# Optimization experiments

Hardware: AMD Instinct MI355X
Metric: run time of the kernel (lower is better)

## Reference

```python
import jax, jax.numpy as jnp
import numpy as np

EPS = 1e-3  # Keras BatchNormalization default epsilon

def _bn(x, g, b, m, v):
    return (x - m) * (g / jnp.sqrt(v + EPS)) + b

def _conv1d(x, w, b):
    # x: [B,T,Cin], w: [K,Cin,Cout], VALID padding
    y = jax.lax.conv_general_dilated(x, w, window_strides=(1,), padding='VALID',
                                     dimension_numbers=('NWC', 'WIO', 'NWC'))
    return y + b

def _lstm(x, W, U, b, return_sequences):
    # Keras LSTM: gates order [i, f, c, o]; sigmoid recurrent act, tanh act
    B, T, _ = x.shape
    H = U.shape[0]
    xz = jnp.einsum('btf,fh->bth', x, W) + b  # precompute input projection [B,T,4H]
    def step(carry, xz_t):
        h, c = carry
        z = xz_t + h @ U
        i, f, g, o = jnp.split(z, 4, axis=-1)
        i = jax.nn.sigmoid(i); f = jax.nn.sigmoid(f)
        g = jnp.tanh(g);       o = jax.nn.sigmoid(o)
        c = f * c + i * g
        h = o * jnp.tanh(c)
        return (h, c), h
    h0 = jnp.zeros((B, H), x.dtype)
    (h_last, _), hs = jax.lax.scan(step, (h0, h0), jnp.swapaxes(xz, 0, 1))
    return jnp.swapaxes(hs, 0, 1) if return_sequences else h_last

def setup_inputs() -> dict:
    key = jax.random.key(0)
    ks = jax.random.split(key, 32)
    B, T, F, C = 4096, 512, 10, 5
    s = 0.1
    d = {}
    d['x'] = jax.random.normal(ks[0], (B, T, F), jnp.float32)
    def bn(i, ch, p):
        d[p + '_g'] = jnp.ones((ch,), jnp.float32) + s * jax.random.normal(ks[i], (ch,))
        d[p + '_b'] = s * jax.random.normal(ks[i + 1], (ch,))
        d[p + '_m'] = s * jax.random.normal(ks[i + 2], (ch,))
        d[p + '_v'] = jnp.ones((ch,), jnp.float32) + 0.05 * jax.random.uniform(ks[i + 3], (ch,))
    bn(1, F, 'bn1'); bn(5, 16, 'bn2'); bn(9, 32, 'bn3')
    d['conv1_w'] = s * jax.random.normal(ks[13], (3, F, 16), jnp.float32)
    d['conv1_b'] = s * jax.random.normal(ks[14], (16,), jnp.float32)
    d['conv2_w'] = s * jax.random.normal(ks[15], (6, 16, 32), jnp.float32)
    d['conv2_b'] = s * jax.random.normal(ks[16], (32,), jnp.float32)
    def lstm_p(i, fin, h, p):
        d[p + '_W'] = s * jax.random.normal(ks[i], (fin, 4 * h), jnp.float32)
        d[p + '_U'] = s * jax.random.normal(ks[i + 1], (h, 4 * h), jnp.float32)
        d[p + '_b'] = s * jax.random.normal(ks[i + 2], (4 * h,), jnp.float32)
    lstm_p(17, 32, 32, 'l1'); lstm_p(20, 32, 24, 'l2'); lstm_p(23, 24, 16, 'l3')
    d['d1_w'] = s * jax.random.normal(ks[26], (16, 8), jnp.float32)
    d['d1_b'] = s * jax.random.normal(ks[27], (8,), jnp.float32)
    d['out_w'] = s * jax.random.normal(ks[28], (8, C), jnp.float32)
    d['out_b'] = s * jax.random.normal(ks[29], (C,), jnp.float32)
    return d

def reference(x, bn1_g, bn1_b, bn1_m, bn1_v, conv1_w, conv1_b,
              bn2_g, bn2_b, bn2_m, bn2_v, conv2_w, conv2_b,
              bn3_g, bn3_b, bn3_m, bn3_v,
              l1_W, l1_U, l1_b, l2_W, l2_U, l2_b, l3_W, l3_U, l3_b,
              d1_w, d1_b, out_w, out_b):
    # inference mode (training=False): BN uses moving stats, dropout is identity
    h = _bn(x, bn1_g, bn1_b, bn1_m, bn1_v)
    h = jax.nn.relu(_conv1d(h, conv1_w, conv1_b))
    h = _bn(h, bn2_g, bn2_b, bn2_m, bn2_v)
    h = jax.nn.relu(_conv1d(h, conv2_w, conv2_b))
    h = _bn(h, bn3_g, bn3_b, bn3_m, bn3_v)
    h = _lstm(h, l1_W, l1_U, l1_b, True)
    h = _lstm(h, l2_W, l2_U, l2_b, True)
    h = _lstm(h, l3_W, l3_U, l3_b, False)  # [B,16]
    h = jax.nn.relu(h @ d1_w + d1_b)
    return jax.nn.softmax(h @ out_w + out_b, axis=-1)
```

## Files before the change

kernel.cpp:

```cpp
#include <hip/hip_runtime.h>
#include <math.h>

#define EPSBN 1e-3f

typedef unsigned long long ull;
typedef __attribute__((ext_vector_type(8))) short bf16x8;
typedef __attribute__((ext_vector_type(4))) float f32x4;

#define WS_W1F 0
#define WS_B1F 480
#define WS_B2F 496
#define WS_W2F 528
#define WS_BL1 3600
#define WS_BL2 3728
#define WS_BL3 3824
#define WS_B1P 3888
#define WS_B2P 7984
#define WS_B3P 11056
#define WS_R2  13104

__device__ __forceinline__ unsigned short f2b(float f) {
  unsigned u = __float_as_uint(f);
  return (unsigned short)((u + 0x7FFFu + ((u >> 16) & 1u)) >> 16);
}
__device__ __forceinline__ float sigm(float v) { return 1.f / (1.f + __expf(-v)); }
__device__ __forceinline__ float tanh_(float v) {
  float e = __expf(-2.f * fabsf(v));
  float t = (1.f - e) / (1.f + e);
  return copysignf(t, v);
}

__global__ __launch_bounds__(256) void prep_kernel(
    const float* __restrict__ bn1g, const float* __restrict__ bn1b,
    const float* __restrict__ bn1m, const float* __restrict__ bn1v,
    const float* __restrict__ bn2g, const float* __restrict__ bn2b,
    const float* __restrict__ bn2m, const float* __restrict__ bn2v,
    const float* __restrict__ bn3g, const float* __restrict__ bn3b,
    const float* __restrict__ bn3m, const float* __restrict__ bn3v,
    const float* __restrict__ c1w, const float* __restrict__ c1b,
    const float* __restrict__ c2w, const float* __restrict__ c2b,
    const float* __restrict__ l1W, const float* __restrict__ l1U, const float* __restrict__ l1b,
    const float* __restrict__ l2W, const float* __restrict__ l2U, const float* __restrict__ l2b,
    const float* __restrict__ l3W, const float* __restrict__ l3U, const float* __restrict__ l3b,
    float* __restrict__ ws)
{
  __shared__ float s1[10], t1[10], s2[16], t2[16], s3[32], t3[32];
  int tid = threadIdx.x;
  if (tid < 10)                  { float s = bn1g[tid] * rsqrtf(bn1v[tid] + EPSBN); s1[tid] = s; t1[tid] = bn1b[tid] - bn1m[tid] * s; }
  else if (tid >= 32 && tid < 48){ int c = tid - 32; float s = bn2g[c] * rsqrtf(bn2v[c] + EPSBN); s2[c] = s; t2[c] = bn2b[c] - bn2m[c] * s; }
  else if (tid >= 64 && tid < 96){ int c = tid - 64; float s = bn3g[c] * rsqrtf(bn3v[c] + EPSBN); s3[c] = s; t3[c] = bn3b[c] - bn3m[c] * s; }
  __syncthreads();

  float* w1f = ws + WS_W1F;
  float* b1f = ws + WS_B1F;
  float* b2f = ws + WS_B2F;
  float* w2f = ws + WS_W2F;
  float* bL1 = ws + WS_BL1;
  float* bL2 = ws + WS_BL2;
  float* bL3 = ws + WS_BL3;
  unsigned short* B1P = (unsigned short*)(ws + WS_B1P);
  unsigned short* B2P = (unsigned short*)(ws + WS_B2P);
  unsigned short* B3P = (unsigned short*)(ws + WS_B3P);

  for (int i = tid; i < 480; i += 256) { int ci = (i >> 4) % 10; w1f[i] = c1w[i] * s1[ci]; }
  for (int co = tid; co < 16; co += 256) {
    float a = c1b[co];
    for (int k = 0; k < 3; k++) for (int ci = 0; ci < 10; ci++) a += t1[ci] * c1w[(k * 10 + ci) * 16 + co];
    b1f[co] = a;
  }
  for (int i = tid; i < 3072; i += 256) { int ci = (i >> 5) & 15; w2f[i] = c2w[i] * s2[ci]; }
  for (int co = tid; co < 32; co += 256) {
    float a = c2b[co];
    for (int k = 0; k < 6; k++) for (int ci = 0; ci < 16; ci++) a += t2[ci] * c2w[(k * 16 + ci) * 32 + co];
    b2f[co] = a;
  }
  for (int j = tid; j < 128; j += 256) {
    float a = l1b[j];
    for (int k = 0; k < 32; k++) a += t3[k] * l1W[k * 128 + j];
    bL1[j] = a;
  }
  for (int j = tid; j < 96; j += 256) bL2[j] = l2b[j];
  for (int j = tid; j < 64; j += 256) bL3[j] = l3b[j];

  for (int i = tid; i < 2 * 8 * 64 * 8; i += 256) {
    int e = i & 7, l = (i >> 3) & 63, nt = (i >> 9) & 7, kt = i >> 12;
    int j = nt * 16 + (l & 15);
    int k = kt * 32 + ((l >> 4) << 3) + e;
    float v = (k < 32) ? l1W[k * 128 + j] * s3[k] : l1U[(k - 32) * 128 + j];
    B1P[i] = f2b(v);
  }
  for (int i = tid; i < 2 * 6 * 64 * 8; i += 256) {
    int e = i & 7, l = (i >> 3) & 63, m = i >> 9;
    int nt = m % 6, kt = m / 6;
    int j = nt * 16 + (l & 15);
    int k = kt * 32 + ((l >> 4) << 3) + e;
    float v = (k < 32) ? l2W[k * 96 + j] : ((k < 56) ? l2U[(k - 32) * 96 + j] : 0.f);
    B2P[i] = f2b(v);
  }
  for (int i = tid; i < 2 * 4 * 64 * 8; i += 256) {
    int e = i & 7, l = (i >> 3) & 63, m = i >> 9;
    int nt = m & 3, kt = m >> 2;
    int j = nt * 16 + (l & 15);
    int k = kt * 32 + ((l >> 4) << 3) + e;
    float v = (k < 24) ? l3W[k * 64 + j] : ((k < 40) ? l3U[(k - 24) * 64 + j] : 0.f);
    B3P[i] = f2b(v);
  }
}

#define CT 128
__global__ __launch_bounds__(256, 4) void conv_kernel(
    const float* __restrict__ x, const float* __restrict__ ws,
    unsigned short* __restrict__ r2, int row0)
{
  int b  = row0 + blockIdx.y;
  int bl = blockIdx.y;
  int t0 = blockIdx.x * CT;
  int n2 = min(CT, 505 - t0);
  int n1 = n2 + 5;
  int nx = n1 + 2;
  int tid = threadIdx.x;

  __shared__ float xs[135 * 10];
  __shared__ float r1s[133 * 17];
  __shared__ float w1f[480];
  __shared__ float b1f[16];
  alignas(16) __shared__ float w2f[3072];
  __shared__ float b2f[32];

  for (int i = tid; i < 480;  i += 256) w1f[i] = ws[WS_W1F + i];
  for (int i = tid; i < 16;   i += 256) b1f[i] = ws[WS_B1F + i];
  for (int i = tid; i < 32;   i += 256) b2f[i] = ws[WS_B2F + i];
  for (int i = tid; i < 3072; i += 256) w2f[i] = ws[WS_W2F + i];
  const float* xb = x + (size_t)b * 512 * 10 + (size_t)t0 * 10;
  for (int i = tid; i < nx * 10; i += 256) xs[i] = xb[i];
  __syncthreads();

  #pragma unroll 1
  for (int i = tid; i < n1 * 16; i += 256) {
    int tt = i >> 4, c = i & 15;
    float a = b1f[c];
    #pragma unroll
    for (int k = 0; k < 3; k++)
      #pragma unroll
      for (int ci = 0; ci < 10; ci++)
        a = fmaf(xs[(tt + k) * 10 + ci], w1f[(k * 10 + ci) * 16 + c], a);
    r1s[tt * 17 + c] = fmaxf(a, 0.f);
  }
  __syncthreads();

  int cog = (tid & 7) * 4;
  int tg  = (tid >> 3) * 4;
  float acc[4][4];
  #pragma unroll
  for (int i2 = 0; i2 < 4; i2++)
    #pragma unroll
    for (int j2 = 0; j2 < 4; j2++) acc[i2][j2] = b2f[cog + j2];
  #pragma unroll 4
  for (int kc = 0; kc < 96; kc++) {
    int k2 = kc >> 4;
    float4 w4 = *(const float4*)&w2f[kc * 32 + cog];
    #pragma unroll
    for (int i2 = 0; i2 < 4; i2++) {
      float xv = r1s[(tg + i2 + k2) * 17 + (kc & 15)];
      acc[i2][0] = fmaf(xv, w4.x, acc[i2][0]);
      acc[i2][1] = fmaf(xv, w4.y, acc[i2][1]);
      acc[i2][2] = fmaf(xv, w4.z, acc[i2][2]);
      acc[i2][3] = fmaf(xv, w4.w, acc[i2][3]);
    }
  }
  #pragma unroll
  for (int i2 = 0; i2 < 4; i2++) {
    int tt = tg + i2;
    if (tt < n2) {
      ull o = (ull)f2b(fmaxf(acc[i2][0], 0.f))
            | ((ull)f2b(fmaxf(acc[i2][1], 0.f)) << 16)
            | ((ull)f2b(fmaxf(acc[i2][2], 0.f)) << 32)
            | ((ull)f2b(fmaxf(acc[i2][3], 0.f)) << 48);
      *(ull*)&r2[((size_t)bl * 505 + (t0 + tt)) * 32 + cog] = o;
    }
  }
}

#define SWZB(row, byte) ((byte) ^ (((row) & 7) << 4))
#define ZST 132

#define MFMA(a, b, c) __builtin_amdgcn_mfma_f32_16x16x32_bf16((a), (b), (c), 0, 0, 0)

__global__ __launch_bounds__(256) void lstm_kernel(
    const unsigned short* __restrict__ r2, const float* __restrict__ ws,
    const float* __restrict__ d1w, const float* __restrict__ d1b,
    const float* __restrict__ outw, const float* __restrict__ outb,
    float* __restrict__ out, int row0)
{
  int tid = threadIdx.x;
  int l   = tid & 63;
  int w   = tid >> 6;
  int r16 = l & 15;
  int g   = l >> 4;
  int rl  = blockIdx.x * 16;

  alignas(16) __shared__ unsigned short xh1[16 * 64];
  alignas(16) __shared__ unsigned short xh2[16 * 64];
  alignas(16) __shared__ unsigned short xh3[16 * 64];
  __shared__ float zbf[16 * ZST];

  const unsigned short* B1P = (const unsigned short*)(ws + WS_B1P);
  const unsigned short* B2P = (const unsigned short*)(ws + WS_B2P);
  const unsigned short* B3P = (const unsigned short*)(ws + WS_B3P);

  int nt1a = 2 * w, nt1b = 2 * w + 1;
  bool has2 = (w < 2);
  int nt2a = has2 ? 2 * w : (2 + w);
  int nt2b = has2 ? 2 * w + 1 : nt2a;
  bf16x8 B1r[2][2], B2r[2][2], B3r[2];
  #pragma unroll
  for (int kt = 0; kt < 2; kt++) {
    B1r[kt][0] = *(const bf16x8*)&B1P[((kt * 8 + nt1a) * 64 + l) * 8];
    B1r[kt][1] = *(const bf16x8*)&B1P[((kt * 8 + nt1b) * 64 + l) * 8];
    B2r[kt][0] = *(const bf16x8*)&B2P[((kt * 6 + nt2a) * 64 + l) * 8];
    B2r[kt][1] = *(const bf16x8*)&B2P[((kt * 6 + nt2b) * 64 + l) * 8];
    B3r[kt]    = *(const bf16x8*)&B3P[((kt * 4 + w) * 64 + l) * 8];
  }
  float b1a = ws[WS_BL1 + nt1a * 16 + r16];
  float b1b = ws[WS_BL1 + nt1b * 16 + r16];
  float b2a = ws[WS_BL2 + nt2a * 16 + r16];
  float b2b = ws[WS_BL2 + nt2b * 16 + r16];
  float b3  = ws[WS_BL3 + w * 16 + r16];

  int u1 = tid & 31, r1a = tid >> 5;
  int s2a = tid, r2a = s2a / 24, u2a = s2a - r2a * 24;
  int s2b = tid + 256, r2b = s2b / 24, u2b = s2b - r2b * 24;
  int u3 = tid & 15, r3a = tid >> 4;
  float c1A = 0.f, c1B = 0.f, c2A = 0.f, c2B = 0.f, c3 = 0.f;

  for (int i = tid; i < 16 * 64; i += 256) { xh1[i] = 0; xh2[i] = 0; xh3[i] = 0; }
  int xrow = tid >> 3, xch = tid & 7;
  const unsigned short* xp = r2 + ((size_t)(rl + xrow) * 505) * 32 + xch * 4;
  ull xreg = 0;
  if (tid < 128) xreg = *(const ull*)xp;
  __syncthreads();
  if (tid < 128) {
    *(ull*)((char*)xh1 + SWZB(xrow, xrow * 128 + xch * 8)) = xreg;
    xreg = *(const ull*)(xp + 32);
  }
  __syncthreads();

  #pragma unroll 1
  for (int t = 0; t < 505; ++t) {
    {
      bf16x8 a0 = *(const bf16x8*)((const char*)xh1 + SWZB(r16, r16 * 128 + g * 16));
      bf16x8 a1 = *(const bf16x8*)((const char*)xh1 + SWZB(r16, r16 * 128 + 64 + g * 16));
      f32x4 acc0 = {b1a, b1a, b1a, b1a};
      f32x4 acc1 = {b1b, b1b, b1b, b1b};
      acc0 = MFMA(a0, B1r[0][0], acc0);
      acc1 = MFMA(a0, B1r[0][1], acc1);
      acc0 = MFMA(a1, B1r[1][0], acc0);
      acc1 = MFMA(a1, B1r[1][1], acc1);
      int c0 = nt1a * 16 + r16, c1c = nt1b * 16 + r16;
      #pragma unroll
      for (int q = 0; q < 4; q++) {
        zbf[(g * 4 + q) * ZST + c0]  = acc0[q];
        zbf[(g * 4 + q) * ZST + c1c] = acc1[q];
      }
    }
    __syncthreads();
    if (tid < 128) {
      if (t < 504) *(ull*)((char*)xh1 + SWZB(xrow, xrow * 128 + xch * 8)) = xreg;
      if (t < 503) xreg = *(const ull*)(xp + (size_t)(t + 2) * 32);
    }
    {
      const float* z = &zbf[r1a * ZST];
      float gi = sigm(z[u1]), gf = sigm(z[32 + u1]), gg = tanh_(z[64 + u1]), go = sigm(z[96 + u1]);
      c1A = fmaf(gf, c1A, gi * gg);
      unsigned short hb = f2b(go * tanh_(c1A));
      *(unsigned short*)((char*)xh1 + SWZB(r1a, r1a * 128 + (32 + u1) * 2)) = hb;
      *(unsigned short*)((char*)xh2 + SWZB(r1a, r1a * 128 + u1 * 2)) = hb;
      int rB = r1a + 8;
      const float* zB = &zbf[rB * ZST];
      gi = sigm(zB[u1]); gf = sigm(zB[32 + u1]); gg = tanh_(zB[64 + u1]); go = sigm(zB[96 + u1]);
      c1B = fmaf(gf, c1B, gi * gg);
      hb = f2b(go * tanh_(c1B));
      *(unsigned short*)((char*)xh1 + SWZB(rB, rB * 128 + (32 + u1) * 2)) = hb;
      *(unsigned short*)((char*)xh2 + SWZB(rB, rB * 128 + u1 * 2)) = hb;
    }
    __syncthreads();
    {
      bf16x8 a0 = *(const bf16x8*)((const char*)xh2 + SWZB(r16, r16 * 128 + g * 16));
      bf16x8 a1 = *(const bf16x8*)((const char*)xh2 + SWZB(r16, r16 * 128 + 64 + g * 16));
      f32x4 acc0 = {b2a, b2a, b2a, b2a};
      acc0 = MFMA(a0, B2r[0][0], acc0);
      acc0 = MFMA(a1, B2r[1][0], acc0);
      int c0 = nt2a * 16 + r16;
      if (has2) {
        f32x4 acc1 = {b2b, b2b, b2b, b2b};
        acc1 = MFMA(a0, B2r[0][1], acc1);
        acc1 = MFMA(a1, B2r[1][1], acc1);
        int c1c = nt2b * 16 + r16;
        #pragma unroll
        for (int q = 0; q < 4; q++) {
          zbf[(g * 4 + q) * ZST + c0]  = acc0[q];
          zbf[(g * 4 + q) * ZST + c1c] = acc1[q];
        }
      } else {
        #pragma unroll
        for (int q = 0; q < 4; q++) zbf[(g * 4 + q) * ZST + c0] = acc0[q];
      }
    }
    __syncthreads();
    {
      const float* z = &zbf[r2a * ZST];
      float gi = sigm(z[u2a]), gf = sigm(z[24 + u2a]), gg = tanh_(z[48 + u2a]), go = sigm(z[72 + u2a]);
      c2A = fmaf(gf, c2A, gi * gg);
      unsigned short hb = f2b(go * tanh_(c2A));
      *(unsigned short*)((char*)xh2 + SWZB(r2a, r2a * 128 + (32 + u2a) * 2)) = hb;
      *(unsigned short*)((char*)xh3 + SWZB(r2a, r2a * 128 + u2a * 2)) = hb;
      if (tid < 128) {
        const float* zB = &zbf[r2b * ZST];
        gi = sigm(zB[u2b]); gf = sigm(zB[24 + u2b]); gg = tanh_(zB[48 + u2b]); go = sigm(zB[72 + u2b]);
        c2B = fmaf(gf, c2B, gi * gg);
        hb = f2b(go * tanh_(c2B));
        *(unsigned short*)((char*)xh2 + SWZB(r2b, r2b * 128 + (32 + u2b) * 2)) = hb;
        *(unsigned short*)((char*)xh3 + SWZB(r2b, r2b * 128 + u2b * 2)) = hb;
      }
    }
    __syncthreads();
    {
      bf16x8 a0 = *(const bf16x8*)((const char*)xh3 + SWZB(r16, r16 * 128 + g * 16));
      bf16x8 a1 = *(const bf16x8*)((const char*)xh3 + SWZB(r16, r16 * 128 + 64 + g * 16));
      f32x4 acc0 = {b3, b3, b3, b3};
      acc0 = MFMA(a0, B3r[0], acc0);
      acc0 = MFMA(a1, B3r[1], acc0);
      int c0 = w * 16 + r16;
      #pragma unroll
      for (int q = 0; q < 4; q++) zbf[(g * 4 + q) * ZST + c0] = acc0[q];
    }
    __syncthreads();
    {
      const float* z = &zbf[r3a * ZST];
      float gi = sigm(z[u3]), gf = sigm(z[16 + u3]), gg = tanh_(z[32 + u3]), go = sigm(z[48 + u3]);
      c3 = fmaf(gf, c3, gi * gg);
      float h = go * tanh_(c3);
      *(unsigned short*)((char*)xh3 + SWZB(r3a, r3a * 128 + (24 + u3) * 2)) = f2b(h);
      zbf[r3a * ZST + 64 + u3] = h;
    }
    __syncthreads();
  }

  if (tid < 16) {
    int row = tid;
    float hd[16];
    #pragma unroll
    for (int u = 0; u < 16; u++) hd[u] = zbf[row * ZST + 64 + u];
    float aa[8];
    #pragma unroll
    for (int o = 0; o < 8; o++) {
      float acc = d1b[o];
      #pragma unroll
      for (int u = 0; u < 16; u++) acc = fmaf(hd[u], d1w[u * 8 + o], acc);
      aa[o] = fmaxf(acc, 0.f);
    }
    float oo[5]; float mx = -1e30f;
    #pragma unroll
    for (int cc = 0; cc < 5; cc++) {
      float acc = outb[cc];
      #pragma unroll
      for (int o = 0; o < 8; o++) acc = fmaf(aa[o], outw[o * 5 + cc], acc);
      oo[cc] = acc; mx = fmaxf(mx, acc);
    }
    float sum = 0.f;
    #pragma unroll
    for (int cc = 0; cc < 5; cc++) { oo[cc] = __expf(oo[cc] - mx); sum += oo[cc]; }
    float inv = 1.f / sum;
    #pragma unroll
    for (int cc = 0; cc < 5; cc++) out[(size_t)(row0 + rl + row) * 5 + cc] = oo[cc] * inv;
  }
}

extern "C" void kernel_launch(void* const* d_in, const int* in_sizes, int n_in,
                              void* d_out, int out_size, void* d_ws, size_t ws_size,
                              hipStream_t stream)
{
  const float* x    = (const float*)d_in[0];
  const float* bn1g = (const float*)d_in[1];
  const float* bn1b = (const float*)d_in[2];
  const float* bn1m = (const float*)d_in[3];
  const float* bn1v = (const float*)d_in[4];
  const float* bn2g = (const float*)d_in[5];
  const float* bn2b = (const float*)d_in[6];
  const float* bn2m = (const float*)d_in[7];
  const float* bn2v = (const float*)d_in[8];
  const float* bn3g = (const float*)d_in[9];
  const float* bn3b = (const float*)d_in[10];
  const float* bn3m = (const float*)d_in[11];
  const float* bn3v = (const float*)d_in[12];
  const float* c1w  = (const float*)d_in[13];
  const float* c1b  = (const float*)d_in[14];
  const float* c2w  = (const float*)d_in[15];
  const float* c2b  = (const float*)d_in[16];
  const float* l1W  = (const float*)d_in[17];
  const float* l1U  = (const float*)d_in[18];
  const float* l1b  = (const float*)d_in[19];
  const float* l2W  = (const float*)d_in[20];
  const float* l2U  = (const float*)d_in[21];
  const float* l2b  = (const float*)d_in[22];
  const float* l3W  = (const float*)d_in[23];
  const float* l3U  = (const float*)d_in[24];
  const float* l3b  = (const float*)d_in[25];
  const float* d1w  = (const float*)d_in[26];
  const float* d1b  = (const float*)d_in[27];
  const float* outw = (const float*)d_in[28];
  const float* outb = (const float*)d_in[29];

  float* ws = (float*)d_ws;
  unsigned short* r2 = (unsigned short*)(ws + WS_R2);

  prep_kernel<<<1, 256, 0, stream>>>(bn1g, bn1b, bn1m, bn1v,
                                     bn2g, bn2b, bn2m, bn2v,
                                     bn3g, bn3b, bn3m, bn3v,
                                     c1w, c1b, c2w, c2b,
                                     l1W, l1U, l1b, l2W, l2U, l2b, l3W, l3U, l3b,
                                     ws);

  size_t availB = (ws_size > (size_t)WS_R2 * 4) ? ws_size - (size_t)WS_R2 * 4 : 0;
  int nch = 1;
  while ((size_t)(4096 / nch) * 505 * 32 * 2 > availB && nch < 16) nch <<= 1;
  int rows_pc = 4096 / nch;

  for (int ch = 0; ch < nch; ++ch) {
    int row0 = ch * rows_pc;
    dim3 cgrid(4, rows_pc);
    conv_kernel<<<cgrid, 256, 0, stream>>>(x, ws, r2, row0);
    lstm_kernel<<<rows_pc / 16, 256, 0, stream>>>(r2, ws, d1w, d1b, outw, outb, (float*)d_out, row0);
  }
}
```

Baseline: 1.311 ms.

## Wavefront-pipeline the three LSTM layers across warps with 4 rows per block

The LSTM kernel now gives each wave one layer: waves 0-1 run layer 1, wave 2 runs layer 2 and wave 3 runs layer 3. The layers are skewed by one timestep, so all three run at once and each step needs two barriers instead of six. Each block now handles 4 batch rows instead of 16, giving four times as many blocks, with launch bounds asking for 4 blocks per CU. The cost is that each MFMA tile only uses 4 of its 16 rows, wasting matrix throughput, and the per-wave work is uneven across layers.

Result: faster. 1.088 ms (-17.0%).

```diff
diff --git a/kernel.cpp b/kernel.cpp
--- a/kernel.cpp
+++ b/kernel.cpp
@@ -28,6 +28,11 @@
   float e = __expf(-2.f * fabsf(v));
   float t = (1.f - e) / (1.f + e);
   return copysignf(t, v);
+}
+__device__ __forceinline__ float gate_h(const float* __restrict__ z, int H, int u, float& c) {
+  float gi = sigm(z[u]), gf = sigm(z[H + u]), gg = tanh_(z[2 * H + u]), go = sigm(z[3 * H + u]);
+  c = fmaf(gf, c, gi * gg);
+  return go * tanh_(c);
 }
 
 __global__ __launch_bounds__(256) void prep_kernel(
@@ -182,11 +187,12 @@
 }
 
 #define SWZB(row, byte) ((byte) ^ (((row) & 7) << 4))
-#define ZST 132
-
 #define MFMA(a, b, c) __builtin_amdgcn_mfma_f32_16x16x32_bf16((a), (b), (c), 0, 0, 0)
-
-__global__ __launch_bounds__(256) void lstm_kernel(
+#define ZST1 132
+#define ZST2 100
+#define ZST3 68
+
+__global__ __launch_bounds__(256, 4) void lstm_kernel(
     const unsigned short* __restrict__ r2, const float* __restrict__ ws,
     const float* __restrict__ d1w, const float* __restrict__ d1b,
     const float* __restrict__ outw, const float* __restrict__ outb,
@@ -197,160 +203,126 @@
   int w   = tid >> 6;
   int r16 = l & 15;
   int g   = l >> 4;
-  int rl  = blockIdx.x * 16;
+  int rl  = blockIdx.x * 4;
 
   alignas(16) __shared__ unsigned short xh1[16 * 64];
   alignas(16) __shared__ unsigned short xh2[16 * 64];
   alignas(16) __shared__ unsigned short xh3[16 * 64];
-  __shared__ float zbf[16 * ZST];
+  __shared__ float zb1[4 * ZST1];
+  __shared__ float zb2[4 * ZST2];
+  __shared__ float zb3[4 * ZST3];
+  __shared__ float hstash[4 * 16];
 
   const unsigned short* B1P = (const unsigned short*)(ws + WS_B1P);
   const unsigned short* B2P = (const unsigned short*)(ws + WS_B2P);
   const unsigned short* B3P = (const unsigned short*)(ws + WS_B3P);
 
-  int nt1a = 2 * w, nt1b = 2 * w + 1;
-  bool has2 = (w < 2);
-  int nt2a = has2 ? 2 * w : (2 + w);
-  int nt2b = has2 ? 2 * w + 1 : nt2a;
-  bf16x8 B1r[2][2], B2r[2][2], B3r[2];
+  const unsigned short* Bp; const float* bbase; const unsigned short* xs8;
+  float* zw; int zst, NJ, jo, ntt;
+  if (w == 0)      { Bp = B1P; bbase = ws + WS_BL1; xs8 = xh1; zw = zb1; zst = ZST1; NJ = 4; jo = 0; ntt = 8; }
+  else if (w == 1) { Bp = B1P; bbase = ws + WS_BL1; xs8 = xh1; zw = zb1; zst = ZST1; NJ = 4; jo = 4; ntt = 8; }
+  else if (w == 2) { Bp = B2P; bbase = ws + WS_BL2; xs8 = xh2; zw = zb2; zst = ZST2; NJ = 6; jo = 0; ntt = 6; }
+  else             { Bp = B3P; bbase = ws + WS_BL3; xs8 = xh3; zw = zb3; zst = ZST3; NJ = 4; jo = 0; ntt = 4; }
+
+  bf16x8 Bfr[12];
+  float barr[6];
   #pragma unroll
-  for (int kt = 0; kt < 2; kt++) {
-    B1r[kt][0] = *(const bf16x8*)&B1P[((kt * 8 + nt1a) * 64 + l) * 8];
-    B1r[kt][1] = *(const bf16x8*)&B1P[((kt * 8 + nt1b) * 64 + l) * 8];
-    B2r[kt][0] = *(const bf16x8*)&B2P[((kt * 6 + nt2a) * 64 + l) * 8];
-    B2r[kt][1] = *(const bf16x8*)&B2P[((kt * 6 + nt2b) * 64 + l) * 8];
-    B3r[kt]    = *(const bf16x8*)&B3P[((kt * 4 + w) * 64 + l) * 8];
-  }
-  float b1a = ws[WS_BL1 + nt1a * 16 + r16];
-  float b1b = ws[WS_BL1 + nt1b * 16 + r16];
-  float b2a = ws[WS_BL2 + nt2a * 16 + r16];
-  float b2b = ws[WS_BL2 + nt2b * 16 + r16];
-  float b3  = ws[WS_BL3 + w * 16 + r16];
-
-  int u1 = tid & 31, r1a = tid >> 5;
-  int s2a = tid, r2a = s2a / 24, u2a = s2a - r2a * 24;
-  int s2b = tid + 256, r2b = s2b / 24, u2b = s2b - r2b * 24;
-  int u3 = tid & 15, r3a = tid >> 4;
-  float c1A = 0.f, c1B = 0.f, c2A = 0.f, c2B = 0.f, c3 = 0.f;
+  for (int j = 0; j < 6; j++) {
+    if (j < NJ) {
+      Bfr[2 * j]     = *(const bf16x8*)&Bp[((0 * ntt + jo + j) * 64 + l) * 8];
+      Bfr[2 * j + 1] = *(const bf16x8*)&Bp[((1 * ntt + jo + j) * 64 + l) * 8];
+      barr[j] = bbase[(jo + j) * 16 + r16];
+    } else {
+      barr[j] = 0.f;
+      Bfr[2 * j] = (bf16x8)0; Bfr[2 * j + 1] = (bf16x8)0;
+    }
+  }
+
+  float cA = 0.f, cB = 0.f;
+  ull xreg = 0;
+  const unsigned short* xp = nullptr;
+  int xrow = 0, xch = 0;
+  if (tid >= 224) {
+    int slot = tid - 224;
+    xrow = slot >> 3; xch = slot & 7;
+    xp = r2 + ((size_t)(rl + xrow) * 505) * 32 + xch * 4;
+    xreg = *(const ull*)xp;
+  }
 
   for (int i = tid; i < 16 * 64; i += 256) { xh1[i] = 0; xh2[i] = 0; xh3[i] = 0; }
-  int xrow = tid >> 3, xch = tid & 7;
-  const unsigned short* xp = r2 + ((size_t)(rl + xrow) * 505) * 32 + xch * 4;
-  ull xreg = 0;
-  if (tid < 128) xreg = *(const ull*)xp;
+  if (tid < 64) hstash[tid] = 0.f;
   __syncthreads();
-  if (tid < 128) {
+  if (tid >= 224) {
     *(ull*)((char*)xh1 + SWZB(xrow, xrow * 128 + xch * 8)) = xreg;
     xreg = *(const ull*)(xp + 32);
   }
   __syncthreads();
 
   #pragma unroll 1
-  for (int t = 0; t < 505; ++t) {
+  for (int i = 0; i < 507; ++i) {
     {
-      bf16x8 a0 = *(const bf16x8*)((const char*)xh1 + SWZB(r16, r16 * 128 + g * 16));
-      bf16x8 a1 = *(const bf16x8*)((const char*)xh1 + SWZB(r16, r16 * 128 + 64 + g * 16));
-      f32x4 acc0 = {b1a, b1a, b1a, b1a};
-      f32x4 acc1 = {b1b, b1b, b1b, b1b};
-      acc0 = MFMA(a0, B1r[0][0], acc0);
-      acc1 = MFMA(a0, B1r[0][1], acc1);
-      acc0 = MFMA(a1, B1r[1][0], acc0);
-      acc1 = MFMA(a1, B1r[1][1], acc1);
-      int c0 = nt1a * 16 + r16, c1c = nt1b * 16 + r16;
+      bf16x8 a0 = *(const bf16x8*)((const char*)xs8 + SWZB(r16, r16 * 128 + g * 16));
+      bf16x8 a1 = *(const bf16x8*)((const char*)xs8 + SWZB(r16, r16 * 128 + 64 + g * 16));
       #pragma unroll
-      for (int q = 0; q < 4; q++) {
-        zbf[(g * 4 + q) * ZST + c0]  = acc0[q];
-        zbf[(g * 4 + q) * ZST + c1c] = acc1[q];
+      for (int j = 0; j < 6; j++) {
+        if (j < NJ) {
+          f32x4 ac = {barr[j], barr[j], barr[j], barr[j]};
+          ac = MFMA(a0, Bfr[2 * j], ac);
+          ac = MFMA(a1, Bfr[2 * j + 1], ac);
+          if (g == 0) {
+            int c = (jo + j) * 16 + r16;
+            #pragma unroll
+            for (int q = 0; q < 4; q++) zw[q * zst + c] = ac[q];
+          }
+        }
       }
     }
     __syncthreads();
-    if (tid < 128) {
-      if (t < 504) *(ull*)((char*)xh1 + SWZB(xrow, xrow * 128 + xch * 8)) = xreg;
-      if (t < 503) xreg = *(const ull*)(xp + (size_t)(t + 2) * 32);
-    }
-    {
-      const float* z = &zbf[r1a * ZST];
-      float gi = sigm(z[u1]), gf = sigm(z[32 + u1]), gg = tanh_(z[64 + u1]), go = sigm(z[96 + u1]);
-      c1A = fmaf(gf, c1A, gi * gg);
-      unsigned short hb = f2b(go * tanh_(c1A));
-      *(unsigned short*)((char*)xh1 + SWZB(r1a, r1a * 128 + (32 + u1) * 2)) = hb;
-      *(unsigned short*)((char*)xh2 + SWZB(r1a, r1a * 128 + u1 * 2)) = hb;
-      int rB = r1a + 8;
-      const float* zB = &zbf[rB * ZST];
-      gi = sigm(zB[u1]); gf = sigm(zB[32 + u1]); gg = tanh_(zB[64 + u1]); go = sigm(zB[96 + u1]);
-      c1B = fmaf(gf, c1B, gi * gg);
-      hb = f2b(go * tanh_(c1B));
-      *(unsigned short*)((char*)xh1 + SWZB(rB, rB * 128 + (32 + u1) * 2)) = hb;
-      *(unsigned short*)((char*)xh2 + SWZB(rB, rB * 128 + u1 * 2)) = hb;
+    if (w < 2) {
+      if (i <= 504) {
+        int s = tid, r = s >> 5, u = s & 31;
+        float h = gate_h(zb1 + r * ZST1, 32, u, cA);
+        unsigned short hb = f2b(h);
+        *(unsigned short*)((char*)xh1 + SWZB(r, r * 128 + (32 + u) * 2)) = hb;
+        *(unsigned short*)((char*)xh2 + SWZB(r, r * 128 + u * 2)) = hb;
+      }
+    } else if (w == 2) {
+      if (i >= 1 && i <= 505) {
+        int s = tid - 128;
+        int r = s / 24, u = s - r * 24;
+        float h = gate_h(zb2 + r * ZST2, 24, u, cA);
+        unsigned short hb = f2b(h);
+        *(unsigned short*)((char*)xh2 + SWZB(r, r * 128 + (32 + u) * 2)) = hb;
+        *(unsigned short*)((char*)xh3 + SWZB(r, r * 128 + u * 2)) = hb;
+        if (tid < 160) {
+          int s2 = tid - 128 + 64;
+          int rB = s2 / 24, uB = s2 - rB * 24;
+          float hB = gate_h(zb2 + rB * ZST2, 24, uB, cB);
+          unsigned short hbB = f2b(hB);
+          *(unsigned short*)((char*)xh2 + SWZB(rB, rB * 128 + (32 + uB) * 2)) = hbB;
+          *(unsigned short*)((char*)xh3 + SWZB(rB, rB * 128 + uB * 2)) = hbB;
+        }
+      }
+    } else {
+      if (i >= 2) {
+        int s = tid - 192, r = s >> 4, u = s & 15;
+        float h = gate_h(zb3 + r * ZST3, 16, u, cA);
+        *(unsigned short*)((char*)xh3 + SWZB(r, r * 128 + (24 + u) * 2)) = f2b(h);
+        hstash[r * 16 + u] = h;
+      }
+      if (tid >= 224) {
+        if (i < 504) *(ull*)((char*)xh1 + SWZB(xrow, xrow * 128 + xch * 8)) = xreg;
+        if (i < 503) xreg = *(const ull*)(xp + (size_t)(i + 2) * 32);
+      }
     }
     __syncthreads();
-    {
-      bf16x8 a0 = *(const bf16x8*)((const char*)xh2 + SWZB(r16, r16 * 128 + g * 16));
-      bf16x8 a1 = *(const bf16x8*)((const char*)xh2 + SWZB(r16, r16 * 128 + 64 + g * 16));
-      f32x4 acc0 = {b2a, b2a, b2a, b2a};
-      acc0 = MFMA(a0, B2r[0][0], acc0);
-      acc0 = MFMA(a1, B2r[1][0], acc0);
-      int c0 = nt2a * 16 + r16;
-      if (has2) {
-        f32x4 acc1 = {b2b, b2b, b2b, b2b};
-        acc1 = MFMA(a0, B2r[0][1], acc1);
-        acc1 = MFMA(a1, B2r[1][1], acc1);
-        int c1c = nt2b * 16 + r16;
-        #pragma unroll
-        for (int q = 0; q < 4; q++) {
-          zbf[(g * 4 + q) * ZST + c0]  = acc0[q];
-          zbf[(g * 4 + q) * ZST + c1c] = acc1[q];
-        }
-      } else {
-        #pragma unroll
-        for (int q = 0; q < 4; q++) zbf[(g * 4 + q) * ZST + c0] = acc0[q];
-      }
-    }
-    __syncthreads();
-    {
-      const float* z = &zbf[r2a * ZST];
-      float gi = sigm(z[u2a]), gf = sigm(z[24 + u2a]), gg = tanh_(z[48 + u2a]), go = sigm(z[72 + u2a]);
-      c2A = fmaf(gf, c2A, gi * gg);
-      unsigned short hb = f2b(go * tanh_(c2A));
-      *(unsigned short*)((char*)xh2 + SWZB(r2a, r2a * 128 + (32 + u2a) * 2)) = hb;
-      *(unsigned short*)((char*)xh3 + SWZB(r2a, r2a * 128 + u2a * 2)) = hb;
-      if (tid < 128) {
-        const float* zB = &zbf[r2b * ZST];
-        gi = sigm(zB[u2b]); gf = sigm(zB[24 + u2b]); gg = tanh_(zB[48 + u2b]); go = sigm(zB[72 + u2b]);
-        c2B = fmaf(gf, c2B, gi * gg);
-        hb = f2b(go * tanh_(c2B));
-        *(unsigned short*)((char*)xh2 + SWZB(r2b, r2b * 128 + (32 + u2b) * 2)) = hb;
-        *(unsigned short*)((char*)xh3 + SWZB(r2b, r2b * 128 + u2b * 2)) = hb;
-      }
-    }
-    __syncthreads();
-    {
-      bf16x8 a0 = *(const bf16x8*)((const char*)xh3 + SWZB(r16, r16 * 128 + g * 16));
-      bf16x8 a1 = *(const bf16x8*)((const char*)xh3 + SWZB(r16, r16 * 128 + 64 + g * 16));
-      f32x4 acc0 = {b3, b3, b3, b3};
-      acc0 = MFMA(a0, B3r[0], acc0);
-      acc0 = MFMA(a1, B3r[1], acc0);
-      int c0 = w * 16 + r16;
-      #pragma unroll
-      for (int q = 0; q < 4; q++) zbf[(g * 4 + q) * ZST + c0] = acc0[q];
-    }
-    __syncthreads();
-    {
-      const float* z = &zbf[r3a * ZST];
-      float gi = sigm(z[u3]), gf = sigm(z[16 + u3]), gg = tanh_(z[32 + u3]), go = sigm(z[48 + u3]);
-      c3 = fmaf(gf, c3, gi * gg);
-      float h = go * tanh_(c3);
-      *(unsigned short*)((char*)xh3 + SWZB(r3a, r3a * 128 + (24 + u3) * 2)) = f2b(h);
-      zbf[r3a * ZST + 64 + u3] = h;
-    }
-    __syncthreads();
-  }
-
-  if (tid < 16) {
+  }
+
+  if (tid < 4) {
     int row = tid;
     float hd[16];
     #pragma unroll
-    for (int u = 0; u < 16; u++) hd[u] = zbf[row * ZST + 64 + u];
+    for (int u = 0; u < 16; u++) hd[u] = hstash[row * 16 + u];
     float aa[8];
     #pragma unroll
     for (int o = 0; o < 8; o++) {
@@ -430,6 +402,6 @@
     int row0 = ch * rows_pc;
     dim3 cgrid(4, rows_pc);
     conv_kernel<<<cgrid, 256, 0, stream>>>(x, ws, r2, row0);
-    lstm_kernel<<<rows_pc / 16, 256, 0, stream>>>(r2, ws, d1w, d1b, outw, outb, (float*)d_out, row0);
-  }
-}
+    lstm_kernel<<<rows_pc / 4, 256, 0, stream>>>(r2, ws, d1w, d1b, outw, outb, (float*)d_out, row0);
+  }
+}
```
